# Optimization experiments

Hardware: AMD Instinct MI355X
Metric: run time of the kernel (lower is better)

Reference implementation:

```python
import jax, jax.numpy as jnp
import numpy as np

N, B, C, IC = 4096, 4, 64, 32  # seq len, batch, in_channels, inter_channels
BN_EPS = 1e-5


def setup_inputs() -> dict:
    key = jax.random.key(0)
    ks = jax.random.split(key, 12)
    s = 0.05
    return {
        "x_thisBranch": jax.random.normal(ks[0], (N, B, C), jnp.float32),
        "x_otherBranch": jax.random.normal(ks[1], (N, B, C), jnp.float32),
        "g_w": jax.random.normal(ks[2], (IC, C), jnp.float32) * s,
        "g_b": jax.random.normal(ks[3], (IC,), jnp.float32) * s,
        "theta_w": jax.random.normal(ks[4], (IC, C), jnp.float32) * s,
        "theta_b": jax.random.normal(ks[5], (IC,), jnp.float32) * s,
        "phi_w": jax.random.normal(ks[6], (IC, C), jnp.float32) * s,
        "phi_b": jax.random.normal(ks[7], (IC,), jnp.float32) * s,
        "wz_w": jax.random.normal(ks[8], (C, IC), jnp.float32) * s,
        "wz_b": jax.random.normal(ks[9], (C,), jnp.float32) * s,
        "bn_gamma": jax.random.normal(ks[10], (C,), jnp.float32) * s + 1.0,
        "bn_beta": jax.random.normal(ks[11], (C,), jnp.float32) * s,
    }


def reference(x_thisBranch, x_otherBranch, g_w, g_b, theta_w, theta_b,
              phi_w, phi_b, wz_w, wz_b, bn_gamma, bn_beta):
    # [N,B,C] -> [B,C,N] as in torch permute(1,2,0)
    xt = jnp.transpose(x_thisBranch, (1, 2, 0))   # (B,C,N)
    xo = jnp.transpose(x_otherBranch, (1, 2, 0))  # (B,C,N)

    # 1x1 conv1d == per-position linear over channels
    g_x = jnp.einsum('ic,bcn->bni', g_w, xt) + g_b            # (B,N,IC)
    theta_x = jnp.einsum('ic,bcn->bin', theta_w, xt) + theta_b[:, None]  # (B,IC,N)
    phi_x = jnp.einsum('ic,bcn->bni', phi_w, xo) + phi_b      # (B,N,IC)

    # f = phi_x @ theta_x : rows indexed by other-branch positions
    f = jnp.einsum('bni,bim->bnm', phi_x, theta_x)            # (B,N,N)
    a = jax.nn.softmax(f, axis=-1)                            # embedded mode

    y = jnp.einsum('bnm,bmi->bni', a, g_x)                    # (B,N,IC)
    y = jnp.transpose(y, (0, 2, 1))                           # (B,IC,N)

    # W_z: 1x1 conv + BatchNorm1d (training-mode batch stats)
    wy = jnp.einsum('ci,bin->bcn', wz_w, y) + wz_b[:, None]   # (B,C,N)
    mean = wy.mean(axis=(0, 2), keepdims=True)
    var = wy.var(axis=(0, 2), keepdims=True)
    wy = (wy - mean) / jnp.sqrt(var + BN_EPS) * bn_gamma[:, None] + bn_beta[:, None]

    return wy + xt
```

## Files before the change

### kernel.cpp

```cpp
#include <hip/hip_runtime.h>
#include <hip/hip_bf16.h>
#include <math.h>

typedef unsigned short ushort_t;
typedef __attribute__((ext_vector_type(8))) short short8;
typedef __attribute__((ext_vector_type(4))) float float4v;

#define NN 4096
#define BB 4
#define CC 64
#define ICH 32

#define OFF_QB 0
#define OFF_KB 262144
#define OFF_VT 524288
#define OFF_OP 786432

static __device__ __forceinline__ ushort_t f2b(float f) {
  union { float f; unsigned u; } v;
  v.f = f;
  return (ushort_t)((v.u + 0x8000u) >> 16);
}
static __device__ __forceinline__ unsigned pack2(float x, float y) {
  return (unsigned)f2b(x) | ((unsigned)f2b(y) << 16);
}
static __device__ __forceinline__ short8 cvt8(const float* p) {
  float4 a = *(const float4*)p;
  float4 b = *(const float4*)(p + 4);
  short8 r;
  r[0] = (short)f2b(a.x); r[1] = (short)f2b(a.y);
  r[2] = (short)f2b(a.z); r[3] = (short)f2b(a.w);
  r[4] = (short)f2b(b.x); r[5] = (short)f2b(b.y);
  r[6] = (short)f2b(b.z); r[7] = (short)f2b(b.w);
  return r;
}

__global__ __launch_bounds__(256) void proj_kernel(
    const float* __restrict__ xt, const float* __restrict__ xo,
    const float* __restrict__ gw, const float* __restrict__ gb,
    const float* __restrict__ tw, const float* __restrict__ tb,
    const float* __restrict__ pw, const float* __restrict__ pb,
    ushort_t* __restrict__ Qb, ushort_t* __restrict__ Kb,
    ushort_t* __restrict__ Vt) {
  __shared__ ushort_t vt_l[ICH * 68];

  int t = threadIdx.x;
  int wv = t >> 6, lane = t & 63, l15 = lane & 15, quad = lane >> 4;
  int b = blockIdx.y, z = blockIdx.z;
  int n0w = blockIdx.x * 64 + wv * 16;

  const float* xsrc = (z == 1) ? xo : xt;
  const float* W = (z == 0) ? tw : (z == 1) ? pw : gw;
  const float* Bv = (z == 0) ? tb : (z == 1) ? pb : gb;
  ushort_t* dst = (z == 0) ? Kb : Qb;

  const float* xr = xsrc + ((size_t)(n0w + l15) * BB + b) * CC;
  short8 a0 = cvt8(xr + quad * 8);
  short8 a1 = cvt8(xr + 32 + quad * 8);

#pragma unroll
  for (int h = 0; h < 2; h++) {
    int i = h * 16 + l15;
    short8 b0 = cvt8(W + (size_t)i * CC + quad * 8);
    short8 b1 = cvt8(W + (size_t)i * CC + 32 + quad * 8);
    float bias = Bv[i];
    float4v acc = {bias, bias, bias, bias};
    acc = __builtin_amdgcn_mfma_f32_16x16x32_bf16(a0, b0, acc, 0, 0, 0);
    acc = __builtin_amdgcn_mfma_f32_16x16x32_bf16(a1, b1, acc, 0, 0, 0);
    if (z < 2) {
#pragma unroll
      for (int r = 0; r < 4; r++)
        dst[((size_t)b * NN + n0w + quad * 4 + r) * ICH + i] = f2b(acc[r]);
    } else {
#pragma unroll
      for (int r = 0; r < 4; r++)
        vt_l[(size_t)i * 68 + wv * 16 + quad * 4 + r] = f2b(acc[r]);
    }
  }
  if (z == 2) {
    __syncthreads();
    int i = t & 31, seg = t >> 5;
    short8 v;
#pragma unroll
    for (int k = 0; k < 8; k++) v[k] = (short)vt_l[i * 68 + seg * 8 + k];
    *(short8*)(Vt + (size_t)(b * ICH + i) * NN + blockIdx.x * 64 + seg * 8) = v;
  }
}

__global__ __launch_bounds__(256) void attn_kernel(
    const ushort_t* __restrict__ Qb, const ushort_t* __restrict__ Kb,
    const ushort_t* __restrict__ Vt, float* __restrict__ OP,
    float* __restrict__ LS, int splits) {
  int t = threadIdx.x;
  int wv = t >> 6, lane = t & 63, l15 = lane & 15, quad = lane >> 4;
  int s = blockIdx.y, b = blockIdx.z;
  int q0 = blockIdx.x * 64 + wv * 16;
  int kspan = NN / splits;

  short8 qf = *(const short8*)(Qb + ((size_t)b * NN + q0 + l15) * ICH + quad * 8);

  float4v o0 = {0.f, 0.f, 0.f, 0.f};
  float4v o1 = {0.f, 0.f, 0.f, 0.f};
  float lsp = 0.f;

  const ushort_t* Kbb = Kb + (size_t)b * NN * ICH;
  const ushort_t* Vtb = Vt + (size_t)b * ICH * NN;
  int mbeg = s * kspan, mend = mbeg + kspan;

  const bool lowq = (quad < 2);
  const bool evenq = ((quad & 1) == 0);

  for (int m0 = mbeg; m0 < mend; m0 += 32) {
    const ushort_t* kp = Kbb + (size_t)(m0 + l15) * ICH + quad * 8;
    short8 kf0 = *(const short8*)(kp);
    short8 kf1 = *(const short8*)(kp + 16 * ICH);
    const ushort_t* vp = Vtb + (size_t)l15 * NN + m0 + quad * 8;
    short8 vf0 = *(const short8*)(vp);
    short8 vf1 = *(const short8*)(vp + 16 * NN);

    float4v z = {0.f, 0.f, 0.f, 0.f};
    float4v st0 = __builtin_amdgcn_mfma_f32_16x16x32_bf16(kf0, qf, z, 0, 0, 0);
    float4v st1 = __builtin_amdgcn_mfma_f32_16x16x32_bf16(kf1, qf, z, 0, 0, 0);

    float p0[4], p1[4];
#pragma unroll
    for (int r = 0; r < 4; r++) {
      p0[r] = __expf(fminf(st0[r], 60.f));
      p1[r] = __expf(fminf(st1[r], 60.f));
      lsp += p0[r] + p1[r];
    }
    unsigned d0 = pack2(p0[0], p0[1]);
    unsigned d1 = pack2(p0[2], p0[3]);
    unsigned d2 = pack2(p1[0], p1[1]);
    unsigned d3 = pack2(p1[2], p1[3]);
    unsigned e0 = lowq ? d2 : d0, e1 = lowq ? d3 : d1;
    unsigned k0 = lowq ? d0 : d2, k1 = lowq ? d1 : d3;
    unsigned r0 = (unsigned)__shfl_xor((int)e0, 32, 64);
    unsigned r1 = (unsigned)__shfl_xor((int)e1, 32, 64);
    unsigned a0 = lowq ? k0 : r0;
    unsigned a1 = lowq ? k1 : r1;
    unsigned a2 = lowq ? r0 : k0;
    unsigned a3 = lowq ? r1 : k1;
    unsigned f0 = evenq ? a2 : a0, f1 = evenq ? a3 : a1;
    unsigned g0 = evenq ? a0 : a2, g1 = evenq ? a1 : a3;
    unsigned s0w = (unsigned)__shfl_xor((int)f0, 16, 64);
    unsigned s1w = (unsigned)__shfl_xor((int)f1, 16, 64);
    unsigned w0 = evenq ? g0 : s0w;
    unsigned w1 = evenq ? g1 : s1w;
    unsigned w2 = evenq ? s0w : g0;
    unsigned w3 = evenq ? s1w : g1;

    union { unsigned u[4]; short8 s8; } pu;
    pu.u[0] = w0; pu.u[1] = w1; pu.u[2] = w2; pu.u[3] = w3;
    short8 pf = pu.s8;

    o0 = __builtin_amdgcn_mfma_f32_16x16x32_bf16(pf, vf0, o0, 0, 0, 0);
    o1 = __builtin_amdgcn_mfma_f32_16x16x32_bf16(pf, vf1, o1, 0, 0, 0);
  }

  lsp += __shfl_xor(lsp, 16, 64);
  lsp += __shfl_xor(lsp, 32, 64);

  size_t base = (size_t)(b * splits + s) * NN;
  if (quad == 0) LS[base + q0 + l15] = lsp;
#pragma unroll
  for (int r = 0; r < 4; r++) {
    int q = q0 + quad * 4 + r;
    float* op = OP + (base + q) * ICH;
    op[l15] = o0[r];
    op[16 + l15] = o1[r];
  }
}

__global__ __launch_bounds__(256) void wz_kernel(
    const float* __restrict__ OP, const float* __restrict__ LS,
    const float* __restrict__ wz_w, const float* __restrict__ wz_b,
    float* __restrict__ WY, float* __restrict__ SP, int splits) {
  __shared__ float yl[64 * 36];
  __shared__ float lsum[64];
  __shared__ float red1[256], red2[256];

  int b = blockIdx.y, n0 = blockIdx.x * 64, t = threadIdx.x;
  int blkid = b * 64 + blockIdx.x;

  if (t < 64) {
    float ssum = 0.f;
    for (int sp = 0; sp < splits; sp++)
      ssum += LS[(size_t)(b * splits + sp) * NN + n0 + t];
    lsum[t] = ssum;
  }
  __syncthreads();
#pragma unroll
  for (int it = 0; it < 8; it++) {
    int lin = it * 256 + t;
    int i = lin & 31, dn = lin >> 5;
    float sacc = 0.f;
    for (int sp = 0; sp < splits; sp++)
      sacc += OP[((size_t)(b * splits + sp) * NN + n0 + dn) * ICH + i];
    yl[dn * 36 + i] = sacc / lsum[dn];
  }
  __syncthreads();

  int c = t >> 2, sub = t & 3;
  float4 w4[8];
#pragma unroll
  for (int j = 0; j < 8; j++) w4[j] = ((const float4*)(wz_w + c * ICH))[j];
  float bc = wz_b[c];
  float s1 = 0.f, s2 = 0.f;
#pragma unroll
  for (int d = 0; d < 16; d++) {
    int dn = sub * 16 + d;
    const float4* y4 = (const float4*)(yl + dn * 36);
    float acc = bc;
#pragma unroll
    for (int j = 0; j < 8; j++) {
      float4 y = y4[j];
      acc += w4[j].x * y.x + w4[j].y * y.y + w4[j].z * y.z + w4[j].w * y.w;
    }
    WY[((size_t)(b * CC + c)) * NN + n0 + dn] = acc;
    s1 += acc;
    s2 += acc * acc;
  }
  red1[t] = s1;
  red2[t] = s2;
  __syncthreads();
  if (t < 64) {
    float a1 = red1[t * 4] + red1[t * 4 + 1] + red1[t * 4 + 2] + red1[t * 4 + 3];
    float a2 = red2[t * 4] + red2[t * 4 + 1] + red2[t * 4 + 2] + red2[t * 4 + 3];
    SP[(size_t)blkid * 64 + t] = a1;
    SP[16384 + (size_t)blkid * 64 + t] = a2;
  }
}

__global__ __launch_bounds__(256) void stats_kernel(
    const float* __restrict__ SP, const float* __restrict__ gamma,
    const float* __restrict__ beta, float* __restrict__ AB) {
  __shared__ double r1[256], r2[256];
  int c = blockIdx.x, t = threadIdx.x;
  r1[t] = (double)SP[(size_t)t * 64 + c];
  r2[t] = (double)SP[16384 + (size_t)t * 64 + c];
  __syncthreads();
  for (int off = 128; off > 0; off >>= 1) {
    if (t < off) {
      r1[t] += r1[t + off];
      r2[t] += r2[t + off];
    }
    __syncthreads();
  }
  if (t == 0) {
    double inv = 1.0 / (double)(BB * NN);
    double mean = r1[0] * inv;
    double var = r2[0] * inv - mean * mean;
    if (var < 0.0) var = 0.0;
    double rstd = 1.0 / sqrt(var + 1e-5);
    float A = gamma[c] * (float)rstd;
    AB[c] = A;
    AB[64 + c] = beta[c] - (float)mean * A;
  }
}

__global__ __launch_bounds__(256) void norm_kernel(
    const float* __restrict__ WY, const float* __restrict__ AB,
    const float* __restrict__ xthis, float* __restrict__ out) {
  __shared__ float xl[64 * 65];
  __shared__ float abr[128];
  int b = blockIdx.y, n0 = blockIdx.x * 64, t = threadIdx.x;
  if (t < 128) abr[t] = AB[t];
#pragma unroll
  for (int it = 0; it < 16; it++) {
    int lin = it * 256 + t;
    int c = lin & 63, dn = lin >> 6;
    xl[dn * 65 + c] = xthis[((size_t)(n0 + dn) * BB + b) * CC + c];
  }
  __syncthreads();
#pragma unroll
  for (int it = 0; it < 16; it++) {
    int lin = it * 256 + t;
    int c = lin >> 6, dn = lin & 63;
    size_t idx = ((size_t)(b * CC + c)) * NN + n0 + dn;
    out[idx] = WY[idx] * abr[c] + abr[64 + c] + xl[dn * 65 + c];
  }
}

extern "C" void kernel_launch(void* const* d_in, const int* in_sizes, int n_in,
                              void* d_out, int out_size, void* d_ws,
                              size_t ws_size, hipStream_t stream) {
  const float* x_this = (const float*)d_in[0];
  const float* x_other = (const float*)d_in[1];
  const float* g_w = (const float*)d_in[2];
  const float* g_b = (const float*)d_in[3];
  const float* th_w = (const float*)d_in[4];
  const float* th_b = (const float*)d_in[5];
  const float* ph_w = (const float*)d_in[6];
  const float* ph_b = (const float*)d_in[7];
  const float* wz_w = (const float*)d_in[8];
  const float* wz_b = (const float*)d_in[9];
  const float* gamma = (const float*)d_in[10];
  const float* beta = (const float*)d_in[11];
  float* out = (float*)d_out;

  float* ws = (float*)d_ws;
  ushort_t* Qb = (ushort_t*)(ws + OFF_QB);
  ushort_t* Kb = (ushort_t*)(ws + OFF_KB);
  ushort_t* Vt = (ushort_t*)(ws + OFF_VT);

  int splits = 4;
  while (splits > 1 &&
         ws_size < (size_t)(786432 + (size_t)splits * 540672 + 32768 +
                            1048576) * 4)
    splits >>= 1;
  float* OP = ws + OFF_OP;
  float* LS = OP + (size_t)splits * 524288;
  float* SP = LS + (size_t)splits * 16384;
  float* WY = SP + 32768;
  float* AB = WY + 1048576;

  hipLaunchKernelGGL(proj_kernel, dim3(NN / 64, BB, 3), dim3(256), 0, stream,
                     x_this, x_other, g_w, g_b, th_w, th_b, ph_w, ph_b,
                     Qb, Kb, Vt);
  hipLaunchKernelGGL(attn_kernel, dim3(NN / 64, splits, BB), dim3(256), 0,
                     stream, Qb, Kb, Vt, OP, LS, splits);
  hipLaunchKernelGGL(wz_kernel, dim3(NN / 64, BB), dim3(256), 0, stream,
                     OP, LS, wz_w, wz_b, WY, SP, splits);
  hipLaunchKernelGGL(stats_kernel, dim3(CC), dim3(256), 0, stream,
                     SP, gamma, beta, AB);
  hipLaunchKernelGGL(norm_kernel, dim3(NN / 64, BB), dim3(256), 0, stream,
                     WY, AB, x_this, out);
}
```

Before: 154.9 us.

## Process four query tiles per wave in attention and stage projection I/O through LDS

The attention kernel now has each wave handle 64 queries (four 16-row fragments), so every K/V fragment load is reused four times. The grid shrinks along the query axis and the key-split count doubles to 8 to keep enough blocks. The projection kernel now stages x and W tiles through shared memory with coalesced float4 loads, and writes Q/K through an LDS transpose as 16-byte stores. The costs are higher register pressure from the 4x2 accumulators and more partial outputs to reduce in wz_kernel because of the extra splits.

```diff
diff --git a/kernel.cpp b/kernel.cpp
--- a/kernel.cpp
+++ b/kernel.cpp
@@ -24,14 +24,10 @@
 static __device__ __forceinline__ unsigned pack2(float x, float y) {
   return (unsigned)f2b(x) | ((unsigned)f2b(y) << 16);
 }
-static __device__ __forceinline__ short8 cvt8(const float* p) {
-  float4 a = *(const float4*)p;
-  float4 b = *(const float4*)(p + 4);
+static __device__ __forceinline__ short8 cvt8lds(const float* p) {
   short8 r;
-  r[0] = (short)f2b(a.x); r[1] = (short)f2b(a.y);
-  r[2] = (short)f2b(a.z); r[3] = (short)f2b(a.w);
-  r[4] = (short)f2b(b.x); r[5] = (short)f2b(b.y);
-  r[6] = (short)f2b(b.z); r[7] = (short)f2b(b.w);
+#pragma unroll
+  for (int j = 0; j < 8; j++) r[j] = (short)f2b(p[j]);
   return r;
 }
 
@@ -42,48 +38,75 @@
     const float* __restrict__ pw, const float* __restrict__ pb,
     ushort_t* __restrict__ Qb, ushort_t* __restrict__ Kb,
     ushort_t* __restrict__ Vt) {
-  __shared__ ushort_t vt_l[ICH * 68];
+  __shared__ float xls[64 * 68];
+  __shared__ float wls[ICH * 68];
+  __shared__ float bls[ICH];
+  __shared__ ushort_t ol[2304];
 
   int t = threadIdx.x;
   int wv = t >> 6, lane = t & 63, l15 = lane & 15, quad = lane >> 4;
   int b = blockIdx.y, z = blockIdx.z;
-  int n0w = blockIdx.x * 64 + wv * 16;
+  int n0 = blockIdx.x * 64;
 
   const float* xsrc = (z == 1) ? xo : xt;
   const float* W = (z == 0) ? tw : (z == 1) ? pw : gw;
   const float* Bv = (z == 0) ? tb : (z == 1) ? pb : gb;
-  ushort_t* dst = (z == 0) ? Kb : Qb;
-
-  const float* xr = xsrc + ((size_t)(n0w + l15) * BB + b) * CC;
-  short8 a0 = cvt8(xr + quad * 8);
-  short8 a1 = cvt8(xr + 32 + quad * 8);
+
+#pragma unroll
+  for (int it = 0; it < 4; it++) {
+    int lin = it * 256 + t;
+    int row = lin >> 4, seg = lin & 15;
+    float4 v = *(const float4*)(xsrc + ((size_t)(n0 + row) * BB + b) * CC + seg * 4);
+    *(float4*)(xls + row * 68 + seg * 4) = v;
+  }
+#pragma unroll
+  for (int it = 0; it < 2; it++) {
+    int lin = it * 256 + t;
+    int row = lin >> 4, seg = lin & 15;
+    float4 v = *(const float4*)(W + (size_t)row * CC + seg * 4);
+    *(float4*)(wls + row * 68 + seg * 4) = v;
+  }
+  if (t < ICH) bls[t] = Bv[t];
+  __syncthreads();
+
+  const float* xr = xls + (wv * 16 + l15) * 68;
+  short8 a0 = cvt8lds(xr + quad * 8);
+  short8 a1 = cvt8lds(xr + 32 + quad * 8);
 
 #pragma unroll
   for (int h = 0; h < 2; h++) {
     int i = h * 16 + l15;
-    short8 b0 = cvt8(W + (size_t)i * CC + quad * 8);
-    short8 b1 = cvt8(W + (size_t)i * CC + 32 + quad * 8);
-    float bias = Bv[i];
+    short8 b0 = cvt8lds(wls + i * 68 + quad * 8);
+    short8 b1 = cvt8lds(wls + i * 68 + 32 + quad * 8);
+    float bias = bls[i];
     float4v acc = {bias, bias, bias, bias};
     acc = __builtin_amdgcn_mfma_f32_16x16x32_bf16(a0, b0, acc, 0, 0, 0);
     acc = __builtin_amdgcn_mfma_f32_16x16x32_bf16(a1, b1, acc, 0, 0, 0);
     if (z < 2) {
 #pragma unroll
       for (int r = 0; r < 4; r++)
-        dst[((size_t)b * NN + n0w + quad * 4 + r) * ICH + i] = f2b(acc[r]);
+        ol[(wv * 16 + quad * 4 + r) * 36 + i] = f2b(acc[r]);
     } else {
 #pragma unroll
       for (int r = 0; r < 4; r++)
-        vt_l[(size_t)i * 68 + wv * 16 + quad * 4 + r] = f2b(acc[r]);
-    }
-  }
-  if (z == 2) {
-    __syncthreads();
+        ol[i * 68 + wv * 16 + quad * 4 + r] = f2b(acc[r]);
+    }
+  }
+  __syncthreads();
+
+  if (z < 2) {
+    ushort_t* dst = (z == 0) ? Kb : Qb;
+    int row = t >> 2, seg = t & 3;
+    short8 v;
+#pragma unroll
+    for (int k = 0; k < 8; k++) v[k] = (short)ol[row * 36 + seg * 8 + k];
+    *(short8*)(dst + ((size_t)b * NN + n0 + row) * ICH + seg * 8) = v;
+  } else {
     int i = t & 31, seg = t >> 5;
     short8 v;
 #pragma unroll
-    for (int k = 0; k < 8; k++) v[k] = (short)vt_l[i * 68 + seg * 8 + k];
-    *(short8*)(Vt + (size_t)(b * ICH + i) * NN + blockIdx.x * 64 + seg * 8) = v;
+    for (int k = 0; k < 8; k++) v[k] = (short)ol[i * 68 + seg * 8 + k];
+    *(short8*)(Vt + (size_t)(b * ICH + i) * NN + n0 + seg * 8) = v;
   }
 }
 
@@ -94,14 +117,22 @@
   int t = threadIdx.x;
   int wv = t >> 6, lane = t & 63, l15 = lane & 15, quad = lane >> 4;
   int s = blockIdx.y, b = blockIdx.z;
-  int q0 = blockIdx.x * 64 + wv * 16;
+  int q0 = blockIdx.x * 256 + wv * 64;
   int kspan = NN / splits;
 
-  short8 qf = *(const short8*)(Qb + ((size_t)b * NN + q0 + l15) * ICH + quad * 8);
-
-  float4v o0 = {0.f, 0.f, 0.f, 0.f};
-  float4v o1 = {0.f, 0.f, 0.f, 0.f};
-  float lsp = 0.f;
+  short8 qf[4];
+#pragma unroll
+  for (int f = 0; f < 4; f++)
+    qf[f] = *(const short8*)(Qb + ((size_t)b * NN + q0 + f * 16 + l15) * ICH +
+                             quad * 8);
+
+  float4v o[4][2];
+#pragma unroll
+  for (int f = 0; f < 4; f++) {
+    o[f][0] = (float4v){0.f, 0.f, 0.f, 0.f};
+    o[f][1] = (float4v){0.f, 0.f, 0.f, 0.f};
+  }
+  float lsp[4] = {0.f, 0.f, 0.f, 0.f};
 
   const ushort_t* Kbb = Kb + (size_t)b * NN * ICH;
   const ushort_t* Vtb = Vt + (size_t)b * ICH * NN;
@@ -118,57 +149,63 @@
     short8 vf0 = *(const short8*)(vp);
     short8 vf1 = *(const short8*)(vp + 16 * NN);
 
-    float4v z = {0.f, 0.f, 0.f, 0.f};
-    float4v st0 = __builtin_amdgcn_mfma_f32_16x16x32_bf16(kf0, qf, z, 0, 0, 0);
-    float4v st1 = __builtin_amdgcn_mfma_f32_16x16x32_bf16(kf1, qf, z, 0, 0, 0);
-
-    float p0[4], p1[4];
+#pragma unroll
+    for (int f = 0; f < 4; f++) {
+      float4v z = {0.f, 0.f, 0.f, 0.f};
+      float4v st0 = __builtin_amdgcn_mfma_f32_16x16x32_bf16(kf0, qf[f], z, 0, 0, 0);
+      float4v st1 = __builtin_amdgcn_mfma_f32_16x16x32_bf16(kf1, qf[f], z, 0, 0, 0);
+
+      float p0[4], p1[4];
+#pragma unroll
+      for (int r = 0; r < 4; r++) {
+        p0[r] = __expf(fminf(st0[r], 60.f));
+        p1[r] = __expf(fminf(st1[r], 60.f));
+        lsp[f] += p0[r] + p1[r];
+      }
+      unsigned d0 = pack2(p0[0], p0[1]);
+      unsigned d1 = pack2(p0[2], p0[3]);
+      unsigned d2 = pack2(p1[0], p1[1]);
+      unsigned d3 = pack2(p1[2], p1[3]);
+      unsigned e0 = lowq ? d2 : d0, e1 = lowq ? d3 : d1;
+      unsigned k0 = lowq ? d0 : d2, k1 = lowq ? d1 : d3;
+      unsigned r0 = (unsigned)__shfl_xor((int)e0, 32, 64);
+      unsigned r1 = (unsigned)__shfl_xor((int)e1, 32, 64);
+      unsigned a0 = lowq ? k0 : r0;
+      unsigned a1 = lowq ? k1 : r1;
+      unsigned a2 = lowq ? r0 : k0;
+      unsigned a3 = lowq ? r1 : k1;
+      unsigned f0 = evenq ? a2 : a0, f1 = evenq ? a3 : a1;
+      unsigned g0 = evenq ? a0 : a2, g1 = evenq ? a1 : a3;
+      unsigned s0w = (unsigned)__shfl_xor((int)f0, 16, 64);
+      unsigned s1w = (unsigned)__shfl_xor((int)f1, 16, 64);
+      unsigned w0 = evenq ? g0 : s0w;
+      unsigned w1 = evenq ? g1 : s1w;
+      unsigned w2 = evenq ? s0w : g0;
+      unsigned w3 = evenq ? s1w : g1;
+
+      union { unsigned u[4]; short8 s8; } pu;
+      pu.u[0] = w0; pu.u[1] = w1; pu.u[2] = w2; pu.u[3] = w3;
+      short8 pf = pu.s8;
+
+      o[f][0] = __builtin_amdgcn_mfma_f32_16x16x32_bf16(pf, vf0, o[f][0], 0, 0, 0);
+      o[f][1] = __builtin_amdgcn_mfma_f32_16x16x32_bf16(pf, vf1, o[f][1], 0, 0, 0);
+    }
+  }
+
+  size_t base = (size_t)(b * splits + s) * NN;
+#pragma unroll
+  for (int f = 0; f < 4; f++) {
+    float v = lsp[f];
+    v += __shfl_xor(v, 16, 64);
+    v += __shfl_xor(v, 32, 64);
+    if (quad == 0) LS[base + q0 + f * 16 + l15] = v;
 #pragma unroll
     for (int r = 0; r < 4; r++) {
-      p0[r] = __expf(fminf(st0[r], 60.f));
-      p1[r] = __expf(fminf(st1[r], 60.f));
-      lsp += p0[r] + p1[r];
-    }
-    unsigned d0 = pack2(p0[0], p0[1]);
-    unsigned d1 = pack2(p0[2], p0[3]);
-    unsigned d2 = pack2(p1[0], p1[1]);
-    unsigned d3 = pack2(p1[2], p1[3]);
-    unsigned e0 = lowq ? d2 : d0, e1 = lowq ? d3 : d1;
-    unsigned k0 = lowq ? d0 : d2, k1 = lowq ? d1 : d3;
-    unsigned r0 = (unsigned)__shfl_xor((int)e0, 32, 64);
-    unsigned r1 = (unsigned)__shfl_xor((int)e1, 32, 64);
-    unsigned a0 = lowq ? k0 : r0;
-    unsigned a1 = lowq ? k1 : r1;
-    unsigned a2 = lowq ? r0 : k0;
-    unsigned a3 = lowq ? r1 : k1;
-    unsigned f0 = evenq ? a2 : a0, f1 = evenq ? a3 : a1;
-    unsigned g0 = evenq ? a0 : a2, g1 = evenq ? a1 : a3;
-    unsigned s0w = (unsigned)__shfl_xor((int)f0, 16, 64);
-    unsigned s1w = (unsigned)__shfl_xor((int)f1, 16, 64);
-    unsigned w0 = evenq ? g0 : s0w;
-    unsigned w1 = evenq ? g1 : s1w;
-    unsigned w2 = evenq ? s0w : g0;
-    unsigned w3 = evenq ? s1w : g1;
-
-    union { unsigned u[4]; short8 s8; } pu;
-    pu.u[0] = w0; pu.u[1] = w1; pu.u[2] = w2; pu.u[3] = w3;
-    short8 pf = pu.s8;
-
-    o0 = __builtin_amdgcn_mfma_f32_16x16x32_bf16(pf, vf0, o0, 0, 0, 0);
-    o1 = __builtin_amdgcn_mfma_f32_16x16x32_bf16(pf, vf1, o1, 0, 0, 0);
-  }
-
-  lsp += __shfl_xor(lsp, 16, 64);
-  lsp += __shfl_xor(lsp, 32, 64);
-
-  size_t base = (size_t)(b * splits + s) * NN;
-  if (quad == 0) LS[base + q0 + l15] = lsp;
-#pragma unroll
-  for (int r = 0; r < 4; r++) {
-    int q = q0 + quad * 4 + r;
-    float* op = OP + (base + q) * ICH;
-    op[l15] = o0[r];
-    op[16 + l15] = o1[r];
+      int q = q0 + f * 16 + quad * 4 + r;
+      float* op = OP + (base + q) * ICH;
+      op[l15] = o[f][0][r];
+      op[16 + l15] = o[f][1][r];
+    }
   }
 }
 
@@ -304,10 +341,10 @@
   ushort_t* Kb = (ushort_t*)(ws + OFF_KB);
   ushort_t* Vt = (ushort_t*)(ws + OFF_VT);
 
-  int splits = 4;
+  int splits = 8;
   while (splits > 1 &&
          ws_size < (size_t)(786432 + (size_t)splits * 540672 + 32768 +
-                            1048576) * 4)
+                            1048576 + 128) * 4)
     splits >>= 1;
   float* OP = ws + OFF_OP;
   float* LS = OP + (size_t)splits * 524288;
@@ -318,7 +355,7 @@
   hipLaunchKernelGGL(proj_kernel, dim3(NN / 64, BB, 3), dim3(256), 0, stream,
                      x_this, x_other, g_w, g_b, th_w, th_b, ph_w, ph_b,
                      Qb, Kb, Vt);
-  hipLaunchKernelGGL(attn_kernel, dim3(NN / 64, splits, BB), dim3(256), 0,
+  hipLaunchKernelGGL(attn_kernel, dim3(NN / 256, splits, BB), dim3(256), 0,
                      stream, Qb, Kb, Vt, OP, LS, splits);
   hipLaunchKernelGGL(wz_kernel, dim3(NN / 64, BB), dim3(256), 0, stream,
                      OP, LS, wz_w, wz_b, WY, SP, splits);
```

Result: faster. 145.7 us (-5.9%).
